# Kernel optimization log

Hardware: AMD Instinct MI355X
Metric: run time of the kernel (lower is better)

The kernel has to match this reference:

```python
import jax, jax.numpy as jnp
import numpy as np

N = 50000       # nodes per type (AMP and Target)
E = 800000      # edges per metapath graph
EP = 200000     # pos/neg supervision edges
H, D = 4, 32    # heads, per-head dim
HID = H * D     # 128 = han_hidden_size * num_heads
HAN_IN = 256
PROT, GEN = 1024, 512
ATT_H = 128     # SemanticAttention hidden


def setup_inputs() -> dict:
    key = jax.random.key(0)
    ks = jax.random.split(key, 24)
    r = lambda i, shape: jax.random.normal(ks[i], shape, jnp.float32) * 0.02
    ri = lambda i, shape: jax.random.randint(ks[i], shape, 0, N, jnp.int32)
    z = lambda shape: jnp.zeros(shape, jnp.float32)
    return {
        "protein_embeddings": jax.random.normal(ks[0], (N, PROT), jnp.float32),
        "genomic_embeddings": jax.random.normal(ks[1], (N, GEN), jnp.float32),
        "W1": r(2, (GEN, HAN_IN)), "b1": z((HAN_IN,)),
        "W2": r(3, (PROT, HAN_IN)), "b2": z((HAN_IN,)),
        "gat_Ws": r(4, (4, HAN_IN, HID)), "gat_bs": z((4, HID)),
        "gat_Wd": r(5, (4, HAN_IN, HID)), "gat_bd": z((4, HID)),
        "gat_attn": r(6, (4, H, D)),
        "p_att_W1": r(7, (HID, ATT_H)), "p_att_b1": z((ATT_H,)), "p_att_W2": r(8, (ATT_H, 1)),
        "g_att_W1": r(9, (HID, ATT_H)), "g_att_b1": z((ATT_H,)), "g_att_W2": r(10, (ATT_H, 1)),
        "pred_W1": r(11, (2 * HID, HID)), "pred_b1": z((HID,)),
        "pred_W2": r(12, (HID, 1)), "pred_b2": z((1,)),
        "e_aa": ri(13, (2, E)), "e_ta": ri(14, (2, E)),
        "e_tt": ri(15, (2, E)), "e_at": ri(16, (2, E)),
        "pos_e": ri(17, (2, EP)), "neg_e": ri(18, (2, EP)),
    }


def gatv2(hs, hd, Ws, bs, Wd, bd, attn, src, dst, n_dst):
    """DGL GATv2Conv (share_weights=False, negative_slope=0.2, activation=relu)."""
    fs = (hs @ Ws + bs).reshape(-1, H, D)  # [Ns,H,D]
    fd = (hd @ Wd + bd).reshape(-1, H, D)  # [Nd,H,D]
    fs_e = fs[src]                          # [E,H,D] gather
    e = jax.nn.leaky_relu(fs_e + fd[dst], negative_slope=0.2)
    logits = jnp.einsum('ehd,hd->eh', e, attn)                 # [E,H]
    m = jax.ops.segment_max(logits, dst, num_segments=n_dst)   # edge-softmax max
    m = jnp.where(jnp.isfinite(m), m, 0.0)                      # zero-in-degree nodes
    ex = jnp.exp(logits - m[dst])
    s = jax.ops.segment_sum(ex, dst, num_segments=n_dst)
    alpha = ex / s[dst]                                         # [E,H]
    out = jax.ops.segment_sum(alpha[:, :, None] * fs_e, dst, num_segments=n_dst)
    return jax.nn.relu(out).reshape(n_dst, HID)                 # flatten(1)


def sem_att(z, Wa, ba, Wo):
    """SemanticAttention: z [N,M,F] -> [N,F]."""
    w = jnp.mean(jnp.tanh(z @ Wa + ba) @ Wo, axis=0)  # [M,1]
    beta = jax.nn.softmax(w, axis=0)[:, 0]            # [M]
    return jnp.einsum('nmf,m->nf', z, beta)


def predict(ha, ht, src, dst, Wp1, bp1, Wp2, bp2):
    h = jnp.concatenate([ha[src], ht[dst]], axis=1)   # [Ep, 2*HID]
    return jax.nn.sigmoid((jax.nn.relu(h @ Wp1 + bp1) @ Wp2 + bp2)[:, 0])


def reference(protein_embeddings, genomic_embeddings, W1, b1, W2, b2,
              gat_Ws, gat_bs, gat_Wd, gat_bd, gat_attn,
              p_att_W1, p_att_b1, p_att_W2, g_att_W1, g_att_b1, g_att_W2,
              pred_W1, pred_b1, pred_W2, pred_b2,
              e_aa, e_ta, e_tt, e_at, pos_e, neg_e):
    # relu_after_w=False branch
    ha = protein_embeddings @ W2 + b2   # AMP node features 'ha'
    ht = genomic_embeddings @ W1 + b1   # Target node features 'ht'
    # metapath 0: AMP->AMP (p group), 1: Target->AMP (p), 2: Target->Target (g), 3: AMP->Target (g)
    z_aa = gatv2(ha, ha, gat_Ws[0], gat_bs[0], gat_Wd[0], gat_bd[0], gat_attn[0], e_aa[0], e_aa[1], N)
    z_ta = gatv2(ht, ha, gat_Ws[1], gat_bs[1], gat_Wd[1], gat_bd[1], gat_attn[1], e_ta[0], e_ta[1], N)
    z_tt = gatv2(ht, ht, gat_Ws[2], gat_bs[2], gat_Wd[2], gat_bd[2], gat_attn[2], e_tt[0], e_tt[1], N)
    z_at = gatv2(ha, ht, gat_Ws[3], gat_bs[3], gat_Wd[3], gat_bd[3], gat_attn[3], e_at[0], e_at[1], N)
    zp = jnp.stack([z_aa, z_ta], axis=1)  # [N,2,HID]
    zg = jnp.stack([z_tt, z_at], axis=1)
    ha_out = sem_att(zp, p_att_W1, p_att_b1, p_att_W2)
    ht_out = sem_att(zg, g_att_W1, g_att_b1, g_att_W2)
    pos = predict(ha_out, ht_out, pos_e[0], pos_e[1], pred_W1, pred_b1, pred_W2, pred_b2)
    neg = predict(ha_out, ht_out, neg_e[0], neg_e[1], pred_W1, pred_b1, pred_W2, pred_b2)
    return (pos, neg)
```

## Files before the change

kernel.cpp:

```cpp
#include <hip/hip_runtime.h>
#include <math.h>

#define N_NODES 50000
#define E_EDGES 800000
#define EP_EDGES 200000
#define NG4 (4 * N_NODES)
#define ETOT (4 * E_EDGES)
#define NBUCK 196

static inline int idiv(int a, int b) { return (a + b - 1) / b; }

typedef short s16x8 __attribute__((ext_vector_type(8)));
typedef float f32x4 __attribute__((ext_vector_type(4)));
typedef unsigned short us;

static __device__ __forceinline__ us f2bf(float f) {
  unsigned int u = __float_as_uint(f);
  u += 0x7FFFu + ((u >> 16) & 1u);
  return (us)(u >> 16);
}
static __device__ __forceinline__ float bflo(unsigned int u) { return __uint_as_float(u << 16); }
static __device__ __forceinline__ float bfhi(unsigned int u) { return __uint_as_float(u & 0xffff0000u); }

__global__ __launch_bounds__(256) void wtrans_all_k(
    const float* __restrict__ W2, const float* __restrict__ W1,
    const float* __restrict__ gWs, const float* __restrict__ gWd,
    const float* __restrict__ prW1, const float* __restrict__ pW1,
    const float* __restrict__ gaW1,
    us* __restrict__ W2t, us* __restrict__ W1t, us* __restrict__ gWst,
    us* __restrict__ gWdt, us* __restrict__ prW1t, us* __restrict__ WaPt,
    us* __restrict__ WaGt)
{
  const float* src; us* dst; int ks, nsh, total;
  switch (blockIdx.z) {
    case 0: src = W2;   dst = W2t;   ks = 10; nsh = 8; total = 262144; break;
    case 1: src = W1;   dst = W1t;   ks = 9;  nsh = 8; total = 131072; break;
    case 2: src = gWs;  dst = gWst;  ks = 8;  nsh = 7; total = 131072; break;
    case 3: src = gWd;  dst = gWdt;  ks = 8;  nsh = 7; total = 131072; break;
    case 4: src = prW1; dst = prW1t; ks = 8;  nsh = 7; total = 32768;  break;
    case 5: src = pW1;  dst = WaPt;  ks = 7;  nsh = 7; total = 16384;  break;
    default: src = gaW1; dst = WaGt; ks = 7;  nsh = 7; total = 16384;  break;
  }
  int psh = ks + nsh;
  int Km1 = (1 << ks) - 1;
  int pm1 = (1 << psh) - 1;
  for (int gid = blockIdx.x * 256 + threadIdx.x; gid < total; gid += gridDim.x * 256) {
    int mat = gid >> psh;
    int rem = gid & pm1;
    int n = rem >> ks, k = rem & Km1;
    dst[gid] = f2bf(src[((size_t)mat << psh) + ((size_t)k << nsh) + n]);
  }
}

__global__ __launch_bounds__(256) void proj2_gemm_k(
    const float* __restrict__ PE, const float* __restrict__ GE,
    const us* __restrict__ W2t, const us* __restrict__ W1t,
    const float* __restrict__ b2, const float* __restrict__ b1,
    us* __restrict__ ha_b, us* __restrict__ ht_b, int M)
{
  const int z = blockIdx.z;
  const float* A = z ? GE : PE;
  const us* Bt = z ? W1t : W2t;
  const float* bias = z ? b1 : b2;
  us* C = z ? ht_b : ha_b;
  const int K = z ? 512 : 1024;

  __shared__ us As[64 * 40];
  __shared__ us Bs[256 * 40];
  const int t = threadIdx.x;
  const int rowBase = blockIdx.x * 64;
  const int srow = t >> 2, skf = (t & 3) * 8;
  const int w = t >> 6, lane = t & 63;
  const int m16 = lane & 15, q = lane >> 4;

  f32x4 acc[4][4];
  const f32x4 zero = {0.f, 0.f, 0.f, 0.f};
#pragma unroll
  for (int i = 0; i < 4; i++)
#pragma unroll
    for (int j = 0; j < 4; j++) acc[i][j] = zero;

  int arow = rowBase + srow;
  if (arow >= M) arow = M - 1;
  const float* aptr = A + (size_t)arow * K;
  const us* bptr = Bt + (size_t)t * K;

  for (int k0 = 0; k0 < K; k0 += 32) {
    const float* ap = aptr + k0 + skf;
    float4 x0 = ((const float4*)ap)[0];
    float4 x1 = ((const float4*)ap)[1];
    uint4 p;
    p.x = (unsigned)f2bf(x0.x) | ((unsigned)f2bf(x0.y) << 16);
    p.y = (unsigned)f2bf(x0.z) | ((unsigned)f2bf(x0.w) << 16);
    p.z = (unsigned)f2bf(x1.x) | ((unsigned)f2bf(x1.y) << 16);
    p.w = (unsigned)f2bf(x1.z) | ((unsigned)f2bf(x1.w) << 16);
    uint4 b0 = ((const uint4*)(bptr + k0))[0];
    uint4 b1v = ((const uint4*)(bptr + k0))[1];
    uint4 b2v = ((const uint4*)(bptr + k0))[2];
    uint4 b3v = ((const uint4*)(bptr + k0))[3];
    ((uint4*)&As[srow * 40 + skf])[0] = p;
    ((uint4*)&Bs[t * 40])[0] = b0;
    ((uint4*)&Bs[t * 40])[1] = b1v;
    ((uint4*)&Bs[t * 40])[2] = b2v;
    ((uint4*)&Bs[t * 40])[3] = b3v;
    __syncthreads();
    s16x8 af[4], bfr[4];
#pragma unroll
    for (int mi = 0; mi < 4; mi++)
      af[mi] = *(const s16x8*)&As[(mi * 16 + m16) * 40 + q * 8];
#pragma unroll
    for (int ni = 0; ni < 4; ni++)
      bfr[ni] = *(const s16x8*)&Bs[(w * 64 + ni * 16 + m16) * 40 + q * 8];
#pragma unroll
    for (int mi = 0; mi < 4; mi++)
#pragma unroll
      for (int ni = 0; ni < 4; ni++)
        acc[mi][ni] = __builtin_amdgcn_mfma_f32_16x16x32_bf16(af[mi], bfr[ni], acc[mi][ni], 0, 0, 0);
    __syncthreads();
  }

#pragma unroll
  for (int ni = 0; ni < 4; ni++) {
    int col = w * 64 + ni * 16 + m16;
    float bcol = bias[col];
#pragma unroll
    for (int mi = 0; mi < 4; mi++) {
#pragma unroll
      for (int r = 0; r < 4; r++) {
        int row = rowBase + mi * 16 + q * 4 + r;
        if (row < M) C[(size_t)row * 256 + col] = f2bf(acc[mi][ni][r] + bcol);
      }
    }
  }
}

__global__ __launch_bounds__(256) void gat_gemm8_k(
    const us* __restrict__ ha, const us* __restrict__ ht,
    const us* __restrict__ gWst, const us* __restrict__ gWdt,
    const float* __restrict__ gbs, const float* __restrict__ gbd,
    us* __restrict__ fs_all, int M)
{
  __shared__ us As[128 * 40];
  __shared__ us Bs[128 * 40];
  const int z = blockIdx.z, g = z >> 1, j = z & 1;
  const us* A = (((j ? 0xC : 0x6) >> g) & 1) ? ht : ha;
  const us* Bt = (j ? gWdt : gWst) + ((size_t)g << 15);
  const float* bias = (j ? gbd : gbs) + g * 128;
  us* C = fs_all + (size_t)z * M * 128;

  const int t = threadIdx.x;
  const int rowBase = blockIdx.y * 128;
  const int srow = t >> 1, sk = (t & 1) * 16;
  const int w = t >> 6, lane = t & 63;
  const int wm = w >> 1, wn = w & 1;
  const int m16 = lane & 15, q = lane >> 4;

  f32x4 acc[4][4];
  const f32x4 zero = {0.f, 0.f, 0.f, 0.f};
#pragma unroll
  for (int i = 0; i < 4; i++)
#pragma unroll
    for (int jj = 0; jj < 4; jj++) acc[i][jj] = zero;

  int arow = rowBase + srow;
  if (arow >= M) arow = M - 1;
  const us* aptr = A + (size_t)arow * 256;
  const us* bptr = Bt + (size_t)srow * 256;

  for (int k0 = 0; k0 < 256; k0 += 32) {
    uint4 a0 = ((const uint4*)(aptr + k0 + sk))[0];
    uint4 a1 = ((const uint4*)(aptr + k0 + sk))[1];
    uint4 b0 = ((const uint4*)(bptr + k0 + sk))[0];
    uint4 b1 = ((const uint4*)(bptr + k0 + sk))[1];
    ((uint4*)&As[srow * 40 + sk])[0] = a0;
    ((uint4*)&As[srow * 40 + sk])[1] = a1;
    ((uint4*)&Bs[srow * 40 + sk])[0] = b0;
    ((uint4*)&Bs[srow * 40 + sk])[1] = b1;
    __syncthreads();
    s16x8 af[4], bfr[4];
#pragma unroll
    for (int mi = 0; mi < 4; mi++)
      af[mi] = *(const s16x8*)&As[(wm * 64 + mi * 16 + m16) * 40 + q * 8];
#pragma unroll
    for (int ni = 0; ni < 4; ni++)
      bfr[ni] = *(const s16x8*)&Bs[(wn * 64 + ni * 16 + m16) * 40 + q * 8];
#pragma unroll
    for (int mi = 0; mi < 4; mi++)
#pragma unroll
      for (int ni = 0; ni < 4; ni++)
        acc[mi][ni] = __builtin_amdgcn_mfma_f32_16x16x32_bf16(af[mi], bfr[ni], acc[mi][ni], 0, 0, 0);
    __syncthreads();
  }

#pragma unroll
  for (int ni = 0; ni < 4; ni++) {
    int col = wn * 64 + ni * 16 + m16;
    float bcol = bias[col];
#pragma unroll
    for (int mi = 0; mi < 4; mi++) {
#pragma unroll
      for (int r = 0; r < 4; r++) {
        int row = rowBase + wm * 64 + mi * 16 + q * 4 + r;
        if (row < M) C[(size_t)row * 128 + col] = f2bf(acc[mi][ni][r] + bcol);
      }
    }
  }
}

__global__ __launch_bounds__(256) void bhist_k(
    const int* __restrict__ e_aa, const int* __restrict__ e_ta,
    const int* __restrict__ e_tt, const int* __restrict__ e_at,
    int* __restrict__ bhist)
{
  int g = blockIdx.z;
  const int* e = g == 0 ? e_aa : g == 1 ? e_ta : g == 2 ? e_tt : e_at;
  const int* dstp = e + E_EDGES;
  __shared__ int lh[256];
  int t = threadIdx.x;
  lh[t] = 0;
  __syncthreads();
  int base = blockIdx.x * 2048;
#pragma unroll
  for (int r = 0; r < 8; r++) {
    int i = base + r * 256 + t;
    if (i < E_EDGES) atomicAdd(&lh[dstp[i] >> 8], 1);
  }
  __syncthreads();
  if (t < NBUCK && lh[t]) atomicAdd(&bhist[g * NBUCK + t], lh[t]);
}

__global__ __launch_bounds__(1024) void bscan_k(const int* __restrict__ bhist,
                                                int* __restrict__ bbase, int* __restrict__ bcur) {
  __shared__ int tmp[1024];
  int t = threadIdx.x;
  int v = (t < 4 * NBUCK) ? bhist[t] : 0;
  tmp[t] = v;
  __syncthreads();
  int x = v;
  for (int d = 1; d < 1024; d <<= 1) {
    int y = (t >= d) ? tmp[t - d] : 0;
    __syncthreads();
    x += y;
    tmp[t] = x;
    __syncthreads();
  }
  if (t < 4 * NBUCK) {
    int e = x - v;
    bbase[t] = e;
    bcur[t] = e;
  }
  if (t == 4 * NBUCK - 1) bbase[4 * NBUCK] = x;
}

__global__ __launch_bounds__(256) void binscatter_k(
    const int* __restrict__ e_aa, const int* __restrict__ e_ta,
    const int* __restrict__ e_tt, const int* __restrict__ e_at,
    int* __restrict__ bcur, unsigned int* __restrict__ epack)
{
  int g = blockIdx.z;
  const int* e = g == 0 ? e_aa : g == 1 ? e_ta : g == 2 ? e_tt : e_at;
  const int* srcp = e;
  const int* dstp = e + E_EDGES;
  const int base = blockIdx.x * 4096;
  const int cnt = min(4096, E_EDGES - base);
  __shared__ int lh[256], sc[256], lcur[256], gb[256];
  __shared__ unsigned int spack[4096];
  __shared__ unsigned short sbuck[4096];
  const int t = threadIdx.x;
  lh[t] = 0;
  __syncthreads();
  int ds[16], ss[16];
#pragma unroll
  for (int r = 0; r < 16; r++) {
    int i = r * 256 + t;
    if (i < cnt) {
      ds[r] = dstp[base + i];
      ss[r] = srcp[base + i];
      atomicAdd(&lh[ds[r] >> 8], 1);
    } else ds[r] = -1;
  }
  __syncthreads();
  int v = lh[t];
  sc[t] = v;
  __syncthreads();
  int x = v;
  for (int d = 1; d < 256; d <<= 1) {
    int y = (t >= d) ? sc[t - d] : 0;
    __syncthreads();
    x += y;
    sc[t] = x;
    __syncthreads();
  }
  lcur[t] = x - v;
  if (t < NBUCK) gb[t] = atomicAdd(&bcur[g * NBUCK + t], v);
  __syncthreads();
#pragma unroll
  for (int r = 0; r < 16; r++) {
    if (ds[r] >= 0) {
      int b = ds[r] >> 8;
      int rank = atomicAdd(&lcur[b], 1);
      spack[rank] = ((unsigned int)ds[r] << 16) | (unsigned int)ss[r];
      sbuck[rank] = (unsigned short)b;
    }
  }
  __syncthreads();
  for (int j = t; j < cnt; j += 256) {
    int b = sbuck[j];
    epack[gb[b] + (j - (sc[b] - lh[b]))] = spack[j];
  }
}

__global__ __launch_bounds__(256) void bucketscatter2_k(
    const int* __restrict__ bbase, const unsigned int* __restrict__ epack,
    int* __restrict__ esrc_all, int* __restrict__ offs4)
{
  int g = blockIdx.z, b = blockIdx.x;
  int gb = g * NBUCK + b;
  int start = bbase[gb], end = bbase[gb + 1];
  int ndst = min(256, N_NODES - (b << 8));
  __shared__ int lh[256], cur[256];
  int t = threadIdx.x;
  lh[t] = 0;
  __syncthreads();
  for (int i = start + t; i < end; i += 256)
    atomicAdd(&lh[(epack[i] >> 16) & 255], 1);
  __syncthreads();
  int v = lh[t];
  cur[t] = v;
  __syncthreads();
  int x = v;
  for (int d = 1; d < 256; d <<= 1) {
    int y = (t >= d) ? cur[t - d] : 0;
    __syncthreads();
    x += y;
    cur[t] = x;
    __syncthreads();
  }
  int mybase = start + x - v;
  if (t < ndst) offs4[g * N_NODES + (b << 8) + t] = mybase;
  cur[t] = mybase;
  __syncthreads();
  if (gb == 4 * NBUCK - 1 && t == 0) offs4[NG4] = end;
  unsigned int pk = (start + t < end) ? epack[start + t] : 0u;
  for (int i = start + t; i < end; i += 256) {
    unsigned int nk = (i + 256 < end) ? epack[i + 256] : 0u;
    int dl = (pk >> 16) & 255;
    int pos = atomicAdd(&cur[dl], 1);
    esrc_all[pos] = (int)(pk & 0xffffu);
    pk = nk;
  }
}

__global__ __launch_bounds__(256) void aggregate4_k(
    const us* __restrict__ fs_all, const float* __restrict__ gattn,
    const int* __restrict__ offs4, const int* __restrict__ esrc_all,
    us* __restrict__ zb_all, int n)
{
  int g = blockIdx.z;
  const us* fs = fs_all + (size_t)(2 * g) * n * 128;
  const us* fd = fs_all + (size_t)(2 * g + 1) * n * 128;
  const float* attn = gattn + g * 128;
  us* zout = zb_all + (size_t)g * n * 128;
  const int* offs = offs4 + (size_t)g * n;

  int node = blockIdx.x * 4 + (threadIdx.x >> 6);
  int lane = threadIdx.x & 63;
  int slot = lane >> 4;
  int sl = lane & 15;
  if (node >= n) return;

  uint4 fdu = *(const uint4*)(fd + (size_t)node * 128 + sl * 8);
  float fdv[8];
  fdv[0] = bflo(fdu.x); fdv[1] = bfhi(fdu.x);
  fdv[2] = bflo(fdu.y); fdv[3] = bfhi(fdu.y);
  fdv[4] = bflo(fdu.z); fdv[5] = bfhi(fdu.z);
  fdv[6] = bflo(fdu.w); fdv[7] = bfhi(fdu.w);
  float4 at0 = *(const float4*)(attn + sl * 8);
  float4 at1 = *(const float4*)(attn + sl * 8 + 4);
  float atv[8] = {at0.x, at0.y, at0.z, at0.w, at1.x, at1.y, at1.z, at1.w};

  int s0 = offs[node], s1 = offs[node + 1];
  float acc[8] = {0.f, 0.f, 0.f, 0.f, 0.f, 0.f, 0.f, 0.f};
  float sacc = 0.f;

  int i = s0 + slot;
  int src = (i < s1) ? esrc_all[i] : 0;
  while (i < s1) {
    int ni = i + 4;
    int nsrc = (ni < s1) ? esrc_all[ni] : 0;
    uint4 fu = *(const uint4*)(fs + (size_t)src * 128 + sl * 8);
    float fv[8];
    fv[0] = bflo(fu.x); fv[1] = bfhi(fu.x);
    fv[2] = bflo(fu.y); fv[3] = bfhi(fu.y);
    fv[4] = bflo(fu.z); fv[5] = bfhi(fu.z);
    fv[6] = bflo(fu.w); fv[7] = bfhi(fu.w);
    float p = 0.f;
#pragma unroll
    for (int j = 0; j < 8; j++) {
      float tt = fv[j] + fdv[j];
      tt = (tt > 0.f) ? tt : 0.2f * tt;
      p += tt * atv[j];
    }
    p += __shfl_xor(p, 1);
    p += __shfl_xor(p, 2);
    float ex = __expf(p);
    sacc += ex;
#pragma unroll
    for (int j = 0; j < 8; j++) acc[j] += ex * fv[j];
    i = ni;
    src = nsrc;
  }

#pragma unroll
  for (int j = 0; j < 8; j++) {
    acc[j] += __shfl_xor(acc[j], 16);
    acc[j] += __shfl_xor(acc[j], 32);
  }
  sacc += __shfl_xor(sacc, 16);
  sacc += __shfl_xor(sacc, 32);

  if (slot == 0) {
    float inv = (s1 > s0) ? (1.f / sacc) : 0.f;
    uint4 o;
    o.x = (unsigned)f2bf(fmaxf(acc[0] * inv, 0.f)) | ((unsigned)f2bf(fmaxf(acc[1] * inv, 0.f)) << 16);
    o.y = (unsigned)f2bf(fmaxf(acc[2] * inv, 0.f)) | ((unsigned)f2bf(fmaxf(acc[3] * inv, 0.f)) << 16);
    o.z = (unsigned)f2bf(fmaxf(acc[4] * inv, 0.f)) | ((unsigned)f2bf(fmaxf(acc[5] * inv, 0.f)) << 16);
    o.w = (unsigned)f2bf(fmaxf(acc[6] * inv, 0.f)) | ((unsigned)f2bf(fmaxf(acc[7] * inv, 0.f)) << 16);
    *(uint4*)(zout + (size_t)node * 128 + sl * 8) = o;
  }
}

__global__ __launch_bounds__(256) void satt_mfma_k(
    const us* __restrict__ z0, const us* __restrict__ z1,
    const us* __restrict__ Wat, const float* __restrict__ ba,
    const float* __restrict__ Wo, float* __restrict__ w_acc, int M)
{
  __shared__ us As[128 * 40];
  __shared__ us Bs[128 * 40];
  const us* Z = blockIdx.z ? z1 : z0;
  const int t = threadIdx.x;
  const int rowBase = blockIdx.y * 128;
  const int srow = t >> 1, sk = (t & 1) * 16;
  const int w = t >> 6, lane = t & 63;
  const int wm = w >> 1, wn = w & 1;
  const int m16 = lane & 15, q = lane >> 4;

  f32x4 acc[4][4];
  const f32x4 zero = {0.f, 0.f, 0.f, 0.f};
#pragma unroll
  for (int i = 0; i < 4; i++)
#pragma unroll
    for (int j = 0; j < 4; j++) acc[i][j] = zero;

  int arow = rowBase + srow;
  if (arow >= M) arow = M - 1;
  const us* aptr = Z + (size_t)arow * 128;
  const us* bptr = Wat + (size_t)srow * 128;

  for (int k0 = 0; k0 < 128; k0 += 32) {
    uint4 a0 = ((const uint4*)(aptr + k0 + sk))[0];
    uint4 a1 = ((const uint4*)(aptr + k0 + sk))[1];
    uint4 b0 = ((const uint4*)(bptr + k0 + sk))[0];
    uint4 b1 = ((const uint4*)(bptr + k0 + sk))[1];
    ((uint4*)&As[srow * 40 + sk])[0] = a0;
    ((uint4*)&As[srow * 40 + sk])[1] = a1;
    ((uint4*)&Bs[srow * 40 + sk])[0] = b0;
    ((uint4*)&Bs[srow * 40 + sk])[1] = b1;
    __syncthreads();
    s16x8 af[4], bfr[4];
#pragma unroll
    for (int mi = 0; mi < 4; mi++)
      af[mi] = *(const s16x8*)&As[(wm * 64 + mi * 16 + m16) * 40 + q * 8];
#pragma unroll
    for (int ni = 0; ni < 4; ni++)
      bfr[ni] = *(const s16x8*)&Bs[(wn * 64 + ni * 16 + m16) * 40 + q * 8];
#pragma unroll
    for (int mi = 0; mi < 4; mi++)
#pragma unroll
      for (int ni = 0; ni < 4; ni++)
        acc[mi][ni] = __builtin_amdgcn_mfma_f32_16x16x32_bf16(af[mi], bfr[ni], acc[mi][ni], 0, 0, 0);
    __syncthreads();
  }

  float s = 0.f;
#pragma unroll
  for (int ni = 0; ni < 4; ni++) {
    int col = wn * 64 + ni * 16 + m16;
    float bcol = ba[col], wcol = Wo[col];
#pragma unroll
    for (int mi = 0; mi < 4; mi++) {
#pragma unroll
      for (int r = 0; r < 4; r++) {
        int row = rowBase + wm * 64 + mi * 16 + q * 4 + r;
        if (row < M) s += tanhf(acc[mi][ni][r] + bcol) * wcol;
      }
    }
  }
  for (int d = 1; d < 64; d <<= 1) s += __shfl_xor(s, d);
  __shared__ float red[4];
  if (lane == 0) red[w] = s;
  __syncthreads();
  if (t == 0) atomicAdd(&w_acc[blockIdx.z], red[0] + red[1] + red[2] + red[3]);
}

__global__ void beta_k(const float* __restrict__ w_acc, float* __restrict__ beta, float invn) {
  if (threadIdx.x == 0 && blockIdx.x == 0) {
    float w0 = w_acc[0] * invn, w1 = w_acc[1] * invn;
    float m = fmaxf(w0, w1);
    float e0 = expf(w0 - m), e1 = expf(w1 - m);
    float s = e0 + e1;
    beta[0] = e0 / s; beta[1] = e1 / s;
    float w2 = w_acc[2] * invn, w3 = w_acc[3] * invn;
    float m2 = fmaxf(w2, w3);
    float e2 = expf(w2 - m2), e3 = expf(w3 - m2);
    float s2 = e2 + e3;
    beta[2] = e2 / s2; beta[3] = e3 / s2;
  }
}

static __device__ __forceinline__ unsigned int comb2(unsigned int a, unsigned int b, float b0, float b1) {
  float lo = bflo(a) * b0 + bflo(b) * b1;
  float hi = bfhi(a) * b0 + bfhi(b) * b1;
  return (unsigned int)f2bf(lo) | ((unsigned int)f2bf(hi) << 16);
}

__global__ __launch_bounds__(256) void combine2_k(const us* __restrict__ zb_all,
                                                  const float* __restrict__ beta,
                                                  us* __restrict__ haob, us* __restrict__ htob, int n8) {
  int z = blockIdx.z;
  const us* za = zb_all + (size_t)(2 * z) * N_NODES * 128;
  const us* zbv = zb_all + (size_t)(2 * z + 1) * N_NODES * 128;
  float b0 = beta[2 * z], b1 = beta[2 * z + 1];
  us* outv = z ? htob : haob;
  for (int i = blockIdx.x * 256 + threadIdx.x; i < n8; i += gridDim.x * 256) {
    uint4 a = ((const uint4*)za)[i];
    uint4 b = ((const uint4*)zbv)[i];
    uint4 o;
    o.x = comb2(a.x, b.x, b0, b1);
    o.y = comb2(a.y, b.y, b0, b1);
    o.z = comb2(a.z, b.z, b0, b1);
    o.w = comb2(a.w, b.w, b0, b1);
    ((uint4*)outv)[i] = o;
  }
}

__global__ __launch_bounds__(256) void pred_fused_k(
    const us* __restrict__ haob, const us* __restrict__ htob,
    const int* __restrict__ pos_e, const int* __restrict__ neg_e,
    const us* __restrict__ prW1t, const float* __restrict__ prb1,
    const float* __restrict__ prW2, const float* __restrict__ prb2,
    float* __restrict__ out, int M)
{
  __shared__ us As[128 * 40];
  __shared__ us Bs[128 * 40];
  const int z = blockIdx.z;
  const int* pe = z ? neg_e : pos_e;
  float* o = out + (size_t)z * M;

  const int t = threadIdx.x;
  const int rowBase = blockIdx.x * 128;
  const int srow = t >> 1, sk = (t & 1) * 16;
  const int w = t >> 6, lane = t & 63;
  const int wm = w >> 1, wn = w & 1;
  const int m16 = lane & 15, q = lane >> 4;

  f32x4 acc[4][4];
  const f32x4 zero = {0.f, 0.f, 0.f, 0.f};
#pragma unroll
  for (int i = 0; i < 4; i++)
#pragma unroll
    for (int j = 0; j < 4; j++) acc[i][j] = zero;

  int arow = rowBase + srow;
  if (arow >= M) arow = M - 1;
  const int srcn = pe[arow];
  const int dstn = pe[M + arow];
  const us* bptr = prW1t + (size_t)srow * 256;

  for (int k0 = 0; k0 < 256; k0 += 32) {
    const us* asrc = (k0 < 128) ? (haob + (size_t)srcn * 128 + k0 + sk)
                                : (htob + (size_t)dstn * 128 + (k0 - 128) + sk);
    uint4 a0 = ((const uint4*)asrc)[0];
    uint4 a1 = ((const uint4*)asrc)[1];
    uint4 b0 = ((const uint4*)(bptr + k0 + sk))[0];
    uint4 b1 = ((const uint4*)(bptr + k0 + sk))[1];
    ((uint4*)&As[srow * 40 + sk])[0] = a0;
    ((uint4*)&As[srow * 40 + sk])[1] = a1;
    ((uint4*)&Bs[srow * 40 + sk])[0] = b0;
    ((uint4*)&Bs[srow * 40 + sk])[1] = b1;
    __syncthreads();
    s16x8 af[4], bfr[4];
#pragma unroll
    for (int mi = 0; mi < 4; mi++)
      af[mi] = *(const s16x8*)&As[(wm * 64 + mi * 16 + m16) * 40 + q * 8];
#pragma unroll
    for (int ni = 0; ni < 4; ni++)
      bfr[ni] = *(const s16x8*)&Bs[(wn * 64 + ni * 16 + m16) * 40 + q * 8];
#pragma unroll
    for (int mi = 0; mi < 4; mi++)
#pragma unroll
      for (int ni = 0; ni < 4; ni++)
        acc[mi][ni] = __builtin_amdgcn_mfma_f32_16x16x32_bf16(af[mi], bfr[ni], acc[mi][ni], 0, 0, 0);
    __syncthreads();
  }

  float* rsum = (float*)As;
  if (t < 128) rsum[t] = 0.f;
  __syncthreads();
  float bcol[4], w2c[4];
#pragma unroll
  for (int ni = 0; ni < 4; ni++) {
    int col = wn * 64 + ni * 16 + m16;
    bcol[ni] = prb1[col];
    w2c[ni] = prW2[col];
  }
#pragma unroll
  for (int mi = 0; mi < 4; mi++) {
#pragma unroll
    for (int r = 0; r < 4; r++) {
      float s = 0.f;
#pragma unroll
      for (int ni = 0; ni < 4; ni++)
        s += fmaxf(acc[mi][ni][r] + bcol[ni], 0.f) * w2c[ni];
      s += __shfl_xor(s, 1);
      s += __shfl_xor(s, 2);
      s += __shfl_xor(s, 4);
      s += __shfl_xor(s, 8);
      if (m16 == 0) atomicAdd(&rsum[wm * 64 + mi * 16 + q * 4 + r], s);
    }
  }
  __syncthreads();
  if (t < 128) {
    int row = rowBase + t;
    if (row < M) o[row] = 1.f / (1.f + expf(-(rsum[t] + prb2[0])));
  }
}

extern "C" void kernel_launch(void* const* d_in, const int* in_sizes, int n_in,
                              void* d_out, int out_size, void* d_ws, size_t ws_size,
                              hipStream_t stream) {
  const float* PE   = (const float*)d_in[0];
  const float* GE   = (const float*)d_in[1];
  const float* W1   = (const float*)d_in[2];
  const float* b1   = (const float*)d_in[3];
  const float* W2   = (const float*)d_in[4];
  const float* b2   = (const float*)d_in[5];
  const float* gWs  = (const float*)d_in[6];
  const float* gbs  = (const float*)d_in[7];
  const float* gWd  = (const float*)d_in[8];
  const float* gbd  = (const float*)d_in[9];
  const float* gattn= (const float*)d_in[10];
  const float* pW1  = (const float*)d_in[11];
  const float* pb1  = (const float*)d_in[12];
  const float* pW2  = (const float*)d_in[13];
  const float* gaW1 = (const float*)d_in[14];
  const float* gab1 = (const float*)d_in[15];
  const float* gaW2 = (const float*)d_in[16];
  const float* prW1 = (const float*)d_in[17];
  const float* prb1 = (const float*)d_in[18];
  const float* prW2 = (const float*)d_in[19];
  const float* prb2 = (const float*)d_in[20];
  const int* e_aa = (const int*)d_in[21];
  const int* e_ta = (const int*)d_in[22];
  const int* e_tt = (const int*)d_in[23];
  const int* e_at = (const int*)d_in[24];
  const int* pos_e = (const int*)d_in[25];
  const int* neg_e = (const int*)d_in[26];
  float* out = (float*)d_out;

  us* usws = (us*)d_ws;
  size_t o = 0;
  us* ha_b   = usws + o; o += (size_t)N_NODES * 256;
  us* ht_b   = usws + o; o += (size_t)N_NODES * 256;
  us* fs_all = usws + o; o += (size_t)8 * N_NODES * 128;
  us* zb_all = usws + o; o += (size_t)4 * N_NODES * 128;
  us* haob   = usws + o; o += (size_t)N_NODES * 128;
  us* htob   = usws + o; o += (size_t)N_NODES * 128;
  us* W2t    = usws + o; o += 262144;
  us* W1t    = usws + o; o += 131072;
  us* gWst   = usws + o; o += 131072;
  us* gWdt   = usws + o; o += 131072;
  us* prW1t  = usws + o; o += 32768;
  us* WaPt   = usws + o; o += 16384;
  us* WaGt   = usws + o; o += 16384;
  float* w_acc = (float*)(usws + o); o += 16;
  float* beta  = w_acc + 4;
  int* ib = (int*)(usws + o);
  size_t io = 0;
  int* bhist = ib + io; io += 1024;
  int* bbase = ib + io; io += 1024;
  int* bcur  = ib + io; io += 1024;
  int* offs4 = ib + io; io += NG4 + 4;
  int* esrc  = ib + io; io += ETOT;
  unsigned int* epack = (unsigned int*)zb_all;

  dim3 blk256(256), blk1024(1024);
  const int MT = idiv(N_NODES, 128);
  const int MT64 = idiv(N_NODES, 64);
  const int ET = idiv(EP_EDGES, 128);

  wtrans_all_k<<<dim3(64, 1, 7), blk256, 0, stream>>>(
      W2, W1, gWs, gWd, prW1, pW1, gaW1, W2t, W1t, gWst, gWdt, prW1t, WaPt, WaGt);

  proj2_gemm_k<<<dim3(MT64, 1, 2), blk256, 0, stream>>>(
      PE, GE, W2t, W1t, b2, b1, ha_b, ht_b, N_NODES);

  gat_gemm8_k<<<dim3(1, MT, 8), blk256, 0, stream>>>(ha_b, ht_b, gWst, gWdt, gbs, gbd, fs_all, N_NODES);

  hipMemsetAsync(bhist, 0, 4 * NBUCK * sizeof(int), stream);
  bhist_k<<<dim3(idiv(E_EDGES, 2048), 1, 4), blk256, 0, stream>>>(e_aa, e_ta, e_tt, e_at, bhist);
  bscan_k<<<1, blk1024, 0, stream>>>(bhist, bbase, bcur);
  binscatter_k<<<dim3(idiv(E_EDGES, 4096), 1, 4), blk256, 0, stream>>>(e_aa, e_ta, e_tt, e_at, bcur, epack);
  bucketscatter2_k<<<dim3(NBUCK, 1, 4), blk256, 0, stream>>>(bbase, epack, esrc, offs4);

  aggregate4_k<<<dim3(idiv(N_NODES, 4), 1, 4), blk256, 0, stream>>>(fs_all, gattn, offs4, esrc, zb_all, N_NODES);

  hipMemsetAsync(w_acc, 0, 4 * sizeof(float), stream);
  satt_mfma_k<<<dim3(1, MT, 2), blk256, 0, stream>>>(
      zb_all, zb_all + (size_t)N_NODES * 128, WaPt, pb1, pW2, w_acc + 0, N_NODES);
  satt_mfma_k<<<dim3(1, MT, 2), blk256, 0, stream>>>(
      zb_all + (size_t)2 * N_NODES * 128, zb_all + (size_t)3 * N_NODES * 128, WaGt, gab1, gaW2, w_acc + 2, N_NODES);
  beta_k<<<1, 64, 0, stream>>>(w_acc, beta, 1.0f / (float)N_NODES);

  combine2_k<<<dim3(2048, 1, 2), blk256, 0, stream>>>(zb_all, beta, haob, htob, N_NODES * 128 / 8);

  pred_fused_k<<<dim3(ET, 1, 2), blk256, 0, stream>>>(
      haob, htob, pos_e, neg_e, prW1t, prb1, prW2, prb2, out, EP_EDGES);
}
```

Baseline: 976.2 us.

## Fold input projections into GAT weights and compute all eight features in one GEMM

Precomputes the combined weights (W2·gat_W and W1·gat_W) and the matching biases on device each call. A single wider GEMM then goes straight from the raw protein and genomic embeddings to all eight per-metapath source and destination feature tensors. This removes the intermediate ha/ht bf16 buffers, their write and re-read, and a separate GEMM launch. In exchange the main GEMM does more arithmetic, since its output width doubles from 256 to 512 over K=1024/512. A naive fp32 weight-combination kernel is added, and rounding now happens on the combined weights rather than on the intermediate activations.

```diff
diff --git a/kernel.cpp b/kernel.cpp
--- a/kernel.cpp
+++ b/kernel.cpp
@@ -22,54 +22,88 @@
 static __device__ __forceinline__ float bflo(unsigned int u) { return __uint_as_float(u << 16); }
 static __device__ __forceinline__ float bfhi(unsigned int u) { return __uint_as_float(u & 0xffff0000u); }
 
-__global__ __launch_bounds__(256) void wtrans_all_k(
+__global__ __launch_bounds__(256) void wtrans3_k(
+    const float* __restrict__ prW1, const float* __restrict__ pW1,
+    const float* __restrict__ gaW1,
+    us* __restrict__ prW1t, us* __restrict__ WaPt, us* __restrict__ WaGt)
+{
+  const float* src; us* dst; int ks, nsh, total;
+  switch (blockIdx.z) {
+    case 0: src = prW1; dst = prW1t; ks = 8; nsh = 7; total = 32768; break;
+    case 1: src = pW1;  dst = WaPt;  ks = 7; nsh = 7; total = 16384; break;
+    default: src = gaW1; dst = WaGt; ks = 7; nsh = 7; total = 16384; break;
+  }
+  int Km1 = (1 << ks) - 1;
+  for (int gid = blockIdx.x * 256 + threadIdx.x; gid < total; gid += gridDim.x * 256) {
+    int n = gid >> ks, k = gid & Km1;
+    dst[gid] = f2bf(src[((size_t)k << nsh) + n]);
+  }
+}
+
+__global__ __launch_bounds__(128) void wcomb_k(
     const float* __restrict__ W2, const float* __restrict__ W1,
     const float* __restrict__ gWs, const float* __restrict__ gWd,
-    const float* __restrict__ prW1, const float* __restrict__ pW1,
-    const float* __restrict__ gaW1,
-    us* __restrict__ W2t, us* __restrict__ W1t, us* __restrict__ gWst,
-    us* __restrict__ gWdt, us* __restrict__ prW1t, us* __restrict__ WaPt,
-    us* __restrict__ WaGt)
-{
-  const float* src; us* dst; int ks, nsh, total;
-  switch (blockIdx.z) {
-    case 0: src = W2;   dst = W2t;   ks = 10; nsh = 8; total = 262144; break;
-    case 1: src = W1;   dst = W1t;   ks = 9;  nsh = 8; total = 131072; break;
-    case 2: src = gWs;  dst = gWst;  ks = 8;  nsh = 7; total = 131072; break;
-    case 3: src = gWd;  dst = gWdt;  ks = 8;  nsh = 7; total = 131072; break;
-    case 4: src = prW1; dst = prW1t; ks = 8;  nsh = 7; total = 32768;  break;
-    case 5: src = pW1;  dst = WaPt;  ks = 7;  nsh = 7; total = 16384;  break;
-    default: src = gaW1; dst = WaGt; ks = 7;  nsh = 7; total = 16384;  break;
-  }
-  int psh = ks + nsh;
-  int Km1 = (1 << ks) - 1;
-  int pm1 = (1 << psh) - 1;
-  for (int gid = blockIdx.x * 256 + threadIdx.x; gid < total; gid += gridDim.x * 256) {
-    int mat = gid >> psh;
-    int rem = gid & pm1;
-    int n = rem >> ks, k = rem & Km1;
-    dst[gid] = f2bf(src[((size_t)mat << psh) + ((size_t)k << nsh) + n]);
-  }
-}
-
-__global__ __launch_bounds__(256) void proj2_gemm_k(
+    us* __restrict__ WcPE, us* __restrict__ WcGE)
+{
+  const int side = blockIdx.z;
+  const int K = side ? 512 : 1024;
+  const int k = blockIdx.x;
+  if (k >= K) return;
+  const int zi = blockIdx.y;
+  const float* Wp = side ? W1 : W2;
+  int sel;
+  if (side == 0) sel = (zi == 0) ? 0 : (zi == 1) ? 4 : (zi == 2) ? 5 : 3;
+  else           sel = (zi == 0) ? 1 : (zi == 1) ? 2 : (zi == 2) ? 6 : 7;
+  const float* Wg = (sel < 4) ? (gWs + (size_t)sel * 32768) : (gWd + (size_t)(sel - 4) * 32768);
+  const int n = threadIdx.x;
+  const float* wrow = Wp + (size_t)k * 256;
+  float s0 = 0.f, s1 = 0.f, s2 = 0.f, s3 = 0.f;
+  for (int m = 0; m < 256; m += 4) {
+    s0 += wrow[m]     * Wg[m * 128 + n];
+    s1 += wrow[m + 1] * Wg[(m + 1) * 128 + n];
+    s2 += wrow[m + 2] * Wg[(m + 2) * 128 + n];
+    s3 += wrow[m + 3] * Wg[(m + 3) * 128 + n];
+  }
+  us* out = side ? WcGE : WcPE;
+  out[((size_t)zi * 128 + n) * K + k] = f2bf((s0 + s1) + (s2 + s3));
+}
+
+__global__ __launch_bounds__(128) void bcomb_k(
+    const float* __restrict__ b2, const float* __restrict__ b1,
+    const float* __restrict__ gWs, const float* __restrict__ gWd,
+    const float* __restrict__ gbs, const float* __restrict__ gbd,
+    float* __restrict__ bcPE, float* __restrict__ bcGE)
+{
+  int t = blockIdx.x * 128 + threadIdx.x;
+  int side = t >> 9, zi = (t >> 7) & 3, n = t & 127;
+  int sel;
+  if (side == 0) sel = (zi == 0) ? 0 : (zi == 1) ? 4 : (zi == 2) ? 5 : 3;
+  else           sel = (zi == 0) ? 1 : (zi == 1) ? 2 : (zi == 2) ? 6 : 7;
+  const float* Wg = (sel < 4) ? (gWs + (size_t)sel * 32768) : (gWd + (size_t)(sel - 4) * 32768);
+  const float* bg = (sel < 4) ? (gbs + sel * 128) : (gbd + (sel - 4) * 128);
+  const float* bp = side ? b1 : b2;
+  float s = bg[n];
+  for (int m = 0; m < 256; m++) s += bp[m] * Wg[m * 128 + n];
+  (side ? bcGE : bcPE)[zi * 128 + n] = s;
+}
+
+__global__ __launch_bounds__(512) void feat8_k(
     const float* __restrict__ PE, const float* __restrict__ GE,
-    const us* __restrict__ W2t, const us* __restrict__ W1t,
-    const float* __restrict__ b2, const float* __restrict__ b1,
-    us* __restrict__ ha_b, us* __restrict__ ht_b, int M)
-{
-  const int z = blockIdx.z;
-  const float* A = z ? GE : PE;
-  const us* Bt = z ? W1t : W2t;
-  const float* bias = z ? b1 : b2;
-  us* C = z ? ht_b : ha_b;
-  const int K = z ? 512 : 1024;
+    const us* __restrict__ WcPE, const us* __restrict__ WcGE,
+    const float* __restrict__ bcPE, const float* __restrict__ bcGE,
+    us* __restrict__ fs_all, int M)
+{
+  const int side = blockIdx.z;
+  const float* A = side ? GE : PE;
+  const us* Bt = side ? WcGE : WcPE;
+  const float* bias = side ? bcGE : bcPE;
+  const int K = side ? 512 : 1024;
 
   __shared__ us As[64 * 40];
-  __shared__ us Bs[256 * 40];
+  __shared__ us Bs[512 * 40];
   const int t = threadIdx.x;
   const int rowBase = blockIdx.x * 64;
-  const int srow = t >> 2, skf = (t & 3) * 8;
+  const int srow = t >> 3, skf = (t & 7) * 4;
   const int w = t >> 6, lane = t & 63;
   const int m16 = lane & 15, q = lane >> 4;
 
@@ -86,19 +120,15 @@
   const us* bptr = Bt + (size_t)t * K;
 
   for (int k0 = 0; k0 < K; k0 += 32) {
-    const float* ap = aptr + k0 + skf;
-    float4 x0 = ((const float4*)ap)[0];
-    float4 x1 = ((const float4*)ap)[1];
-    uint4 p;
+    float4 x0 = *(const float4*)(aptr + k0 + skf);
+    uint2 p;
     p.x = (unsigned)f2bf(x0.x) | ((unsigned)f2bf(x0.y) << 16);
     p.y = (unsigned)f2bf(x0.z) | ((unsigned)f2bf(x0.w) << 16);
-    p.z = (unsigned)f2bf(x1.x) | ((unsigned)f2bf(x1.y) << 16);
-    p.w = (unsigned)f2bf(x1.z) | ((unsigned)f2bf(x1.w) << 16);
     uint4 b0 = ((const uint4*)(bptr + k0))[0];
     uint4 b1v = ((const uint4*)(bptr + k0))[1];
     uint4 b2v = ((const uint4*)(bptr + k0))[2];
     uint4 b3v = ((const uint4*)(bptr + k0))[3];
-    ((uint4*)&As[srow * 40 + skf])[0] = p;
+    *(uint2*)&As[srow * 40 + skf] = p;
     ((uint4*)&Bs[t * 40])[0] = b0;
     ((uint4*)&Bs[t * 40])[1] = b1v;
     ((uint4*)&Bs[t * 40])[2] = b2v;
@@ -119,88 +149,20 @@
     __syncthreads();
   }
 
+  const int zi = w >> 1;
+  int zslot;
+  if (side == 0) zslot = (zi == 0) ? 0 : (zi == 1) ? 1 : (zi == 2) ? 3 : 6;
+  else           zslot = (zi == 0) ? 2 : (zi == 1) ? 4 : (zi == 2) ? 5 : 7;
+  us* C = fs_all + (size_t)zslot * M * 128;
 #pragma unroll
   for (int ni = 0; ni < 4; ni++) {
-    int col = w * 64 + ni * 16 + m16;
-    float bcol = bias[col];
+    int col = (w & 1) * 64 + ni * 16 + m16;
+    float bcol = bias[zi * 128 + col];
 #pragma unroll
     for (int mi = 0; mi < 4; mi++) {
 #pragma unroll
       for (int r = 0; r < 4; r++) {
         int row = rowBase + mi * 16 + q * 4 + r;
-        if (row < M) C[(size_t)row * 256 + col] = f2bf(acc[mi][ni][r] + bcol);
-      }
-    }
-  }
-}
-
-__global__ __launch_bounds__(256) void gat_gemm8_k(
-    const us* __restrict__ ha, const us* __restrict__ ht,
-    const us* __restrict__ gWst, const us* __restrict__ gWdt,
-    const float* __restrict__ gbs, const float* __restrict__ gbd,
-    us* __restrict__ fs_all, int M)
-{
-  __shared__ us As[128 * 40];
-  __shared__ us Bs[128 * 40];
-  const int z = blockIdx.z, g = z >> 1, j = z & 1;
-  const us* A = (((j ? 0xC : 0x6) >> g) & 1) ? ht : ha;
-  const us* Bt = (j ? gWdt : gWst) + ((size_t)g << 15);
-  const float* bias = (j ? gbd : gbs) + g * 128;
-  us* C = fs_all + (size_t)z * M * 128;
-
-  const int t = threadIdx.x;
-  const int rowBase = blockIdx.y * 128;
-  const int srow = t >> 1, sk = (t & 1) * 16;
-  const int w = t >> 6, lane = t & 63;
-  const int wm = w >> 1, wn = w & 1;
-  const int m16 = lane & 15, q = lane >> 4;
-
-  f32x4 acc[4][4];
-  const f32x4 zero = {0.f, 0.f, 0.f, 0.f};
-#pragma unroll
-  for (int i = 0; i < 4; i++)
-#pragma unroll
-    for (int jj = 0; jj < 4; jj++) acc[i][jj] = zero;
-
-  int arow = rowBase + srow;
-  if (arow >= M) arow = M - 1;
-  const us* aptr = A + (size_t)arow * 256;
-  const us* bptr = Bt + (size_t)srow * 256;
-
-  for (int k0 = 0; k0 < 256; k0 += 32) {
-    uint4 a0 = ((const uint4*)(aptr + k0 + sk))[0];
-    uint4 a1 = ((const uint4*)(aptr + k0 + sk))[1];
-    uint4 b0 = ((const uint4*)(bptr + k0 + sk))[0];
-    uint4 b1 = ((const uint4*)(bptr + k0 + sk))[1];
-    ((uint4*)&As[srow * 40 + sk])[0] = a0;
-    ((uint4*)&As[srow * 40 + sk])[1] = a1;
-    ((uint4*)&Bs[srow * 40 + sk])[0] = b0;
-    ((uint4*)&Bs[srow * 40 + sk])[1] = b1;
-    __syncthreads();
-    s16x8 af[4], bfr[4];
-#pragma unroll
-    for (int mi = 0; mi < 4; mi++)
-      af[mi] = *(const s16x8*)&As[(wm * 64 + mi * 16 + m16) * 40 + q * 8];
-#pragma unroll
-    for (int ni = 0; ni < 4; ni++)
-      bfr[ni] = *(const s16x8*)&Bs[(wn * 64 + ni * 16 + m16) * 40 + q * 8];
-#pragma unroll
-    for (int mi = 0; mi < 4; mi++)
-#pragma unroll
-      for (int ni = 0; ni < 4; ni++)
-        acc[mi][ni] = __builtin_amdgcn_mfma_f32_16x16x32_bf16(af[mi], bfr[ni], acc[mi][ni], 0, 0, 0);
-    __syncthreads();
-  }
-
-#pragma unroll
-  for (int ni = 0; ni < 4; ni++) {
-    int col = wn * 64 + ni * 16 + m16;
-    float bcol = bias[col];
-#pragma unroll
-    for (int mi = 0; mi < 4; mi++) {
-#pragma unroll
-      for (int r = 0; r < 4; r++) {
-        int row = rowBase + wm * 64 + mi * 16 + q * 4 + r;
         if (row < M) C[(size_t)row * 128 + col] = f2bf(acc[mi][ni][r] + bcol);
       }
     }
@@ -670,19 +632,17 @@
 
   us* usws = (us*)d_ws;
   size_t o = 0;
-  us* ha_b   = usws + o; o += (size_t)N_NODES * 256;
-  us* ht_b   = usws + o; o += (size_t)N_NODES * 256;
   us* fs_all = usws + o; o += (size_t)8 * N_NODES * 128;
   us* zb_all = usws + o; o += (size_t)4 * N_NODES * 128;
   us* haob   = usws + o; o += (size_t)N_NODES * 128;
   us* htob   = usws + o; o += (size_t)N_NODES * 128;
-  us* W2t    = usws + o; o += 262144;
-  us* W1t    = usws + o; o += 131072;
-  us* gWst   = usws + o; o += 131072;
-  us* gWdt   = usws + o; o += 131072;
+  us* WcPE   = usws + o; o += 524288;
+  us* WcGE   = usws + o; o += 262144;
   us* prW1t  = usws + o; o += 32768;
   us* WaPt   = usws + o; o += 16384;
   us* WaGt   = usws + o; o += 16384;
+  float* bcPE = (float*)(usws + o); o += 1024;
+  float* bcGE = (float*)(usws + o); o += 1024;
   float* w_acc = (float*)(usws + o); o += 16;
   float* beta  = w_acc + 4;
   int* ib = (int*)(usws + o);
@@ -694,18 +654,16 @@
   int* esrc  = ib + io; io += ETOT;
   unsigned int* epack = (unsigned int*)zb_all;
 
-  dim3 blk256(256), blk1024(1024);
+  dim3 blk128(128), blk256(256), blk512(512), blk1024(1024);
   const int MT = idiv(N_NODES, 128);
   const int MT64 = idiv(N_NODES, 64);
   const int ET = idiv(EP_EDGES, 128);
 
-  wtrans_all_k<<<dim3(64, 1, 7), blk256, 0, stream>>>(
-      W2, W1, gWs, gWd, prW1, pW1, gaW1, W2t, W1t, gWst, gWdt, prW1t, WaPt, WaGt);
-
-  proj2_gemm_k<<<dim3(MT64, 1, 2), blk256, 0, stream>>>(
-      PE, GE, W2t, W1t, b2, b1, ha_b, ht_b, N_NODES);
-
-  gat_gemm8_k<<<dim3(1, MT, 8), blk256, 0, stream>>>(ha_b, ht_b, gWst, gWdt, gbs, gbd, fs_all, N_NODES);
+  wcomb_k<<<dim3(1024, 4, 2), blk128, 0, stream>>>(W2, W1, gWs, gWd, WcPE, WcGE);
+  bcomb_k<<<dim3(8), blk128, 0, stream>>>(b2, b1, gWs, gWd, gbs, gbd, bcPE, bcGE);
+  wtrans3_k<<<dim3(32, 1, 3), blk256, 0, stream>>>(prW1, pW1, gaW1, prW1t, WaPt, WaGt);
+
+  feat8_k<<<dim3(MT64, 1, 2), blk512, 0, stream>>>(PE, GE, WcPE, WcGE, bcPE, bcGE, fs_all, N_NODES);
 
   hipMemsetAsync(bhist, 0, 4 * NBUCK * sizeof(int), stream);
   bhist_k<<<dim3(idiv(E_EDGES, 2048), 1, 4), blk256, 0, stream>>>(e_aa, e_ta, e_tt, e_at, bhist);
```

New measurement: 1.061 ms. +8.7%, slower.
